# Performance work log

Hardware: AMD Instinct MI355X
Metric: run time of the kernel (lower is better)

## Reference

```python
import jax, jax.numpy as jnp
import numpy as np

B, C, H, W = 16, 512, 64, 64


def setup_inputs() -> dict:
    key = jax.random.key(0)
    ks = jax.random.split(key, 8)
    s = 1.0 / np.sqrt(C)  # fan-in scale like torch conv default
    return {
        "x": jax.random.normal(ks[0], (B, C, H, W), dtype=jnp.float32),
        "y": jax.random.normal(ks[1], (B, C), dtype=jnp.float32),
        "wq": jax.random.normal(ks[2], (C, C), dtype=jnp.float32) * s,
        "bq": jax.random.normal(ks[3], (C,), dtype=jnp.float32) * s,
        "wk": jax.random.normal(ks[4], (C, C), dtype=jnp.float32) * s,
        "bk": jax.random.normal(ks[5], (C,), dtype=jnp.float32) * s,
        "wv": jax.random.normal(ks[6], (C, C), dtype=jnp.float32) * s,
        "bv": jax.random.normal(ks[7], (C,), dtype=jnp.float32) * s,
        "gamma": jnp.ones((1,), dtype=jnp.float32),
    }


def _conv1x1_flat(inp_flat, w, b):
    # inp_flat: (B, C, N); 1x1 conv == per-pixel channel GEMM
    return jnp.einsum("oc,bcn->bon", w, inp_flat) + b[None, :, None]


def reference(x, y, wq, bq, wk, bk, wv, bv, gamma):
    b, c, h, w = x.shape
    n = h * w
    # align=True: y (B, C) broadcast to (B, C, H, W); flatten spatial dims
    y_flat = jnp.broadcast_to(y[:, :, None], (b, c, n))
    x_flat = x.reshape(b, c, n)
    # exchange=False: q = y, k = v = x
    pq = _conv1x1_flat(y_flat, wq, bq)          # (B, C, N)
    pk = _conv1x1_flat(x_flat, wk, bk)          # (B, C, N)
    pv = _conv1x1_flat(x_flat, wv, bv)          # (B, C, N)
    energy = jnp.einsum("bcn,bdn->bcd", pq, pk)  # (B, C, C) channel attention
    attn = jax.nn.softmax(energy, axis=-1)
    out = jnp.einsum("bcd,bdn->bcn", attn, pv)   # (B, C, N)
    out = out.reshape(b, c, h, w)
    return gamma * out + x
```

## Files before the change

kernel.cpp:

```cpp
#include <hip/hip_runtime.h>
#include <hip/hip_bf16.h>

#define Bn 16
#define Cn 512
#define Nn 4096

typedef unsigned short u16;
typedef __bf16 bf16x8 __attribute__((ext_vector_type(8)));
typedef float f32x4 __attribute__((ext_vector_type(4)));
typedef unsigned short u16x8 __attribute__((ext_vector_type(8)));

__device__ __forceinline__ u16 f2bf(float f) {
    __hip_bfloat16 h = __float2bfloat16(f);
    return *reinterpret_cast<u16*>(&h);
}

__device__ __forceinline__ void glds16(const u16* g, u16* l) {
    __builtin_amdgcn_global_load_lds(
        (const __attribute__((address_space(1))) void*)g,
        (__attribute__((address_space(3))) void*)l, 16, 0, 0);
}

__global__ __launch_bounds__(256) void k_transpose(
    const float* __restrict__ x, u16* __restrict__ xt, float* __restrict__ sxp)
{
    __shared__ float tile[128 * 65];
    const int b = blockIdx.z, c0 = blockIdx.y * 128, n0 = blockIdx.x * 64;
    const int t = threadIdx.x;
    const float* xb = x + ((size_t)(b * Cn + c0)) * Nn + n0;

    float part[8];
#pragma unroll
    for (int r = 0; r < 8; ++r) {
        int cl = (t >> 4) + r * 16;
        int nl = (t & 15) * 4;
        float4 v = *(const float4*)(xb + (size_t)cl * Nn + nl);
        float* tp = &tile[cl * 65 + nl];
        tp[0] = v.x; tp[1] = v.y; tp[2] = v.z; tp[3] = v.w;
        part[r] = (v.x + v.y) + (v.z + v.w);
    }
#pragma unroll
    for (int m = 1; m < 16; m <<= 1) {
#pragma unroll
        for (int r = 0; r < 8; ++r) part[r] += __shfl_xor(part[r], m);
    }
    if ((t & 15) == 0) {
#pragma unroll
        for (int r = 0; r < 8; ++r) {
            int cl = (t >> 4) + r * 16;
            sxp[(size_t)(b * Cn + c0 + cl) * 64 + blockIdx.x] = part[r];
        }
    }
    __syncthreads();
    u16* xtb = xt + ((size_t)(b * Nn + n0)) * Cn + c0;
#pragma unroll
    for (int r = 0; r < 4; ++r) {
        int nl = (t >> 4) + r * 16;
        int c8 = (t & 15) * 8;
        u16x8 hv;
#pragma unroll
        for (int i = 0; i < 8; ++i) hv[i] = f2bf(tile[(c8 + i) * 65 + nl]);
        *(u16x8*)(xtb + (size_t)nl * Cn + c8) = hv;
    }
}

__global__ __launch_bounds__(256) void k_sxred(
    const float* __restrict__ sxp, float* __restrict__ sx)
{
    int i = blockIdx.x * 256 + threadIdx.x;
    const float4* p = (const float4*)(sxp + (size_t)i * 64);
    float s = 0.f;
#pragma unroll
    for (int j = 0; j < 16; ++j) {
        float4 v = p[j];
        s += (v.x + v.y) + (v.z + v.w);
    }
    sx[i] = s;
}

__global__ __launch_bounds__(256) void k_qk(
    const float* __restrict__ wq, const float* __restrict__ bq,
    const float* __restrict__ wk, const float* __restrict__ bk,
    const float* __restrict__ y, const float* __restrict__ sx,
    float* __restrict__ qy, float* __restrict__ sk)
{
    const int w = threadIdx.x >> 6, lane = threadIdx.x & 63;
    const int o = blockIdx.x * 4 + w;
    const int b = blockIdx.y;
    const int mode = blockIdx.z;
    const float* W = mode ? wk : wq;
    const float* vec = mode ? (sx + b * Cn) : (y + b * Cn);
    float sum = 0.f;
#pragma unroll
    for (int i = 0; i < 8; ++i) {
        int k2 = lane + i * 64;
        sum += W[(size_t)o * Cn + k2] * vec[k2];
    }
#pragma unroll
    for (int m = 1; m < 64; m <<= 1) sum += __shfl_xor(sum, m);
    if (lane == 0) {
        if (mode) sk[b * Cn + o] = sum + 4096.0f * bk[o];
        else      qy[b * Cn + o] = sum + bq[o];
    }
}

__global__ __launch_bounds__(256) void k_wvt(
    const float* __restrict__ wv, u16* __restrict__ wvt)
{
    __shared__ float tl[64 * 65];
    const int d0 = blockIdx.x * 64, e0 = blockIdx.y * 64;
    const int t = threadIdx.x;
#pragma unroll
    for (int r = 0; r < 4; ++r) {
        int d = (t >> 4) + r * 16, e4 = (t & 15) * 4;
        float4 v = *(const float4*)(wv + (size_t)(d0 + d) * Cn + e0 + e4);
        float* p = &tl[d * 65 + e4];
        p[0] = v.x; p[1] = v.y; p[2] = v.z; p[3] = v.w;
    }
    __syncthreads();
#pragma unroll
    for (int r = 0; r < 4; ++r) {
        int e = (t >> 4) + r * 16, d4 = (t & 15) * 4;
        ushort4 h;
        h.x = f2bf(tl[(d4 + 0) * 65 + e]);
        h.y = f2bf(tl[(d4 + 1) * 65 + e]);
        h.z = f2bf(tl[(d4 + 2) * 65 + e]);
        h.w = f2bf(tl[(d4 + 3) * 65 + e]);
        *(ushort4*)(wvt + (size_t)(e0 + e) * Cn + d0 + d4) = h;
    }
}

__global__ __launch_bounds__(256) void k_softmax(
    const float* __restrict__ qy, const float* __restrict__ sk,
    const float* __restrict__ bv, u16* __restrict__ attn,
    float* __restrict__ beff)
{
    __shared__ float red[4], red2[4], red3[4];
    const int b = blockIdx.x >> 9, c = blockIdx.x & 511;
    const int t = threadIdx.x;
    const float q = qy[b * Cn + c];
    const float l0 = q * sk[b * Cn + t];
    const float l1 = q * sk[b * Cn + t + 256];
    float mx = fmaxf(l0, l1);
#pragma unroll
    for (int m = 1; m < 64; m <<= 1) mx = fmaxf(mx, __shfl_xor(mx, m));
    if ((t & 63) == 0) red[t >> 6] = mx;
    __syncthreads();
    mx = fmaxf(fmaxf(red[0], red[1]), fmaxf(red[2], red[3]));
    const float e0 = __expf(l0 - mx), e1 = __expf(l1 - mx);
    float s = e0 + e1;
#pragma unroll
    for (int m = 1; m < 64; m <<= 1) s += __shfl_xor(s, m);
    if ((t & 63) == 0) red2[t >> 6] = s;
    __syncthreads();
    s = red2[0] + red2[1] + red2[2] + red2[3];
    const float inv = 1.0f / s;
    const float a0 = e0 * inv, a1 = e1 * inv;
    u16* arow = attn + ((size_t)(b * Cn + c)) * Cn;
    arow[t] = f2bf(a0);
    arow[t + 256] = f2bf(a1);
    float pb = a0 * bv[t] + a1 * bv[t + 256];
#pragma unroll
    for (int m = 1; m < 64; m <<= 1) pb += __shfl_xor(pb, m);
    if ((t & 63) == 0) red3[t >> 6] = pb;
    __syncthreads();
    if (t == 0) beff[b * Cn + c] = red3[0] + red3[1] + red3[2] + red3[3];
}

template <int FINAL>
__global__ __launch_bounds__(256) void k_gemm(
    const u16* __restrict__ A, size_t strideA,
    const u16* __restrict__ Bt, size_t strideB,
    int N,
    u16* __restrict__ outBf, size_t strideOb,
    float* __restrict__ outF,
    const float* __restrict__ xres,
    const float* __restrict__ beff,
    const float* __restrict__ gamma)
{
    constexpr int K = 512;
    __shared__ u16 la[128 * 32];
    __shared__ u16 lb[128 * 32];
    const int b = blockIdx.z;
    const int m0 = blockIdx.y * 128;
    const int n0 = blockIdx.x * 128;
    A  += (size_t)b * strideA;
    Bt += (size_t)b * strideB;
    const int t = threadIdx.x;
    const int lane = t & 63;
    const int w = t >> 6;
    const int wm = (w >> 1) * 64, wn = (w & 1) * 64;
    const int l15 = lane & 15, quad = lane >> 4;

    f32x4 acc[4][4];
#pragma unroll
    for (int i = 0; i < 4; ++i)
#pragma unroll
        for (int j = 0; j < 4; ++j)
            acc[i][j] = (f32x4){0.f, 0.f, 0.f, 0.f};

    const int rb = w * 16;
    const int lrow = lane >> 2;
    const int lcol = (lane & 3) * 8;

    for (int k0 = 0; k0 < K; k0 += 32) {
        __syncthreads();
        const u16* gA = A + (size_t)(m0 + rb + lrow) * K + k0 + lcol;
        glds16(gA, &la[rb * 32]);
        glds16(gA + (size_t)64 * K, &la[(rb + 64) * 32]);
        const u16* gB = Bt + (size_t)(n0 + rb + lrow) * K + k0 + lcol;
        glds16(gB, &lb[rb * 32]);
        glds16(gB + (size_t)64 * K, &lb[(rb + 64) * 32]);
        __syncthreads();

        bf16x8 af[4], bfr[4];
#pragma unroll
        for (int mi = 0; mi < 4; ++mi)
            af[mi] = *(const bf16x8*)&la[(wm + mi * 16 + l15) * 32 + quad * 8];
#pragma unroll
        for (int ni = 0; ni < 4; ++ni)
            bfr[ni] = *(const bf16x8*)&lb[(wn + ni * 16 + l15) * 32 + quad * 8];
#pragma unroll
        for (int mi = 0; mi < 4; ++mi)
#pragma unroll
            for (int ni = 0; ni < 4; ++ni)
                acc[mi][ni] = __builtin_amdgcn_mfma_f32_16x16x32_bf16(
                    af[mi], bfr[ni], acc[mi][ni], 0, 0, 0);
    }

    if (FINAL) {
        const float g = gamma[0];
#pragma unroll
        for (int mi = 0; mi < 4; ++mi) {
#pragma unroll
            for (int reg = 0; reg < 4; ++reg) {
                const int r = m0 + wm + mi * 16 + quad * 4 + reg;
                const float be = beff[b * Cn + r];
                const size_t base = ((size_t)(b * Cn + r)) * N;
#pragma unroll
                for (int ni = 0; ni < 4; ++ni) {
                    const int cidx = n0 + wn + ni * 16 + l15;
                    outF[base + cidx] = g * (acc[mi][ni][reg] + be) + xres[base + cidx];
                }
            }
        }
    } else {
#pragma unroll
        for (int mi = 0; mi < 4; ++mi) {
#pragma unroll
            for (int reg = 0; reg < 4; ++reg) {
                const int r = m0 + wm + mi * 16 + quad * 4 + reg;
                const size_t base = (size_t)b * strideOb + (size_t)r * N;
#pragma unroll
                for (int ni = 0; ni < 4; ++ni) {
                    const int cidx = n0 + wn + ni * 16 + l15;
                    outBf[base + cidx] = f2bf(acc[mi][ni][reg]);
                }
            }
        }
    }
}

extern "C" void kernel_launch(void* const* d_in, const int* in_sizes, int n_in,
                              void* d_out, int out_size, void* d_ws, size_t ws_size,
                              hipStream_t stream)
{
    const float* x     = (const float*)d_in[0];
    const float* y     = (const float*)d_in[1];
    const float* wq    = (const float*)d_in[2];
    const float* bq    = (const float*)d_in[3];
    const float* wk    = (const float*)d_in[4];
    const float* bk    = (const float*)d_in[5];
    const float* wv    = (const float*)d_in[6];
    const float* bv    = (const float*)d_in[7];
    const float* gamma = (const float*)d_in[8];
    float* out = (float*)d_out;

    char* ws = (char*)d_ws;
    u16*   xt   = (u16*)  (ws + 0);
    float* sxp  = (float*)(ws + 67108864);
    float* sx   = (float*)(ws + 69206016);
    float* qy   = (float*)(ws + 69238784);
    float* sk   = (float*)(ws + 69271552);
    float* beff = (float*)(ws + 69304320);
    u16*   attn = (u16*)  (ws + 69337088);
    u16*   wvt  = (u16*)  (ws + 77725696);
    u16*   weff = (u16*)  (ws + 78249984);

    k_transpose<<<dim3(64, 4, Bn), dim3(256), 0, stream>>>(x, xt, sxp);
    k_sxred<<<dim3(32), dim3(256), 0, stream>>>(sxp, sx);
    k_wvt<<<dim3(8, 8), dim3(256), 0, stream>>>(wv, wvt);
    k_qk<<<dim3(128, Bn, 2), dim3(256), 0, stream>>>(wq, bq, wk, bk, y, sx, qy, sk);
    k_softmax<<<dim3(Bn * Cn), dim3(256), 0, stream>>>(qy, sk, bv, attn, beff);
    k_gemm<0><<<dim3(4, 4, Bn), dim3(256), 0, stream>>>(
        attn, (size_t)Cn * Cn, wvt, (size_t)0, Cn,
        weff, (size_t)Cn * Cn, nullptr, nullptr, nullptr, nullptr);
    k_gemm<1><<<dim3(32, 4, Bn), dim3(256), 0, stream>>>(
        weff, (size_t)Cn * Cn, xt, (size_t)Nn * Cn, Nn,
        nullptr, (size_t)0, out, x, beff, gamma);
}
```

Before: 361.1 us.

## Double K-tile depth with XOR-swizzled LDS and stage final epilogue through LDS

```diff
diff --git a/kernel.cpp b/kernel.cpp
--- a/kernel.cpp
+++ b/kernel.cpp
@@ -179,8 +179,9 @@
     const float* __restrict__ gamma)
 {
     constexpr int K = 512;
-    __shared__ u16 la[128 * 32];
-    __shared__ u16 lb[128 * 32];
+    __shared__ float smem_f[8448];
+    u16* la = (u16*)smem_f;
+    u16* lb = la + 128 * 64;
     const int b = blockIdx.z;
     const int m0 = blockIdx.y * 128;
     const int n0 = blockIdx.x * 128;
@@ -199,49 +200,78 @@
         for (int j = 0; j < 4; ++j)
             acc[i][j] = (f32x4){0.f, 0.f, 0.f, 0.f};
 
-    const int rb = w * 16;
-    const int lrow = lane >> 2;
-    const int lcol = (lane & 3) * 8;
-
-    for (int k0 = 0; k0 < K; k0 += 32) {
+    const int srow8 = lane >> 3;
+    const int lgcol = ((lane & 7) ^ srow8) * 8;
+
+    for (int k0 = 0; k0 < K; k0 += 64) {
         __syncthreads();
-        const u16* gA = A + (size_t)(m0 + rb + lrow) * K + k0 + lcol;
-        glds16(gA, &la[rb * 32]);
-        glds16(gA + (size_t)64 * K, &la[(rb + 64) * 32]);
-        const u16* gB = Bt + (size_t)(n0 + rb + lrow) * K + k0 + lcol;
-        glds16(gB, &lb[rb * 32]);
-        glds16(gB + (size_t)64 * K, &lb[(rb + 64) * 32]);
+#pragma unroll
+        for (int j = 0; j < 4; ++j) {
+            const int row = w * 32 + j * 8 + srow8;
+            const int sb = (w * 256 + j * 64) * 8;
+            glds16(A  + (size_t)(m0 + row) * K + k0 + lgcol, la + sb);
+            glds16(Bt + (size_t)(n0 + row) * K + k0 + lgcol, lb + sb);
+        }
         __syncthreads();
 
-        bf16x8 af[4], bfr[4];
-#pragma unroll
-        for (int mi = 0; mi < 4; ++mi)
-            af[mi] = *(const bf16x8*)&la[(wm + mi * 16 + l15) * 32 + quad * 8];
-#pragma unroll
-        for (int ni = 0; ni < 4; ++ni)
-            bfr[ni] = *(const bf16x8*)&lb[(wn + ni * 16 + l15) * 32 + quad * 8];
-#pragma unroll
-        for (int mi = 0; mi < 4; ++mi)
-#pragma unroll
-            for (int ni = 0; ni < 4; ++ni)
-                acc[mi][ni] = __builtin_amdgcn_mfma_f32_16x16x32_bf16(
-                    af[mi], bfr[ni], acc[mi][ni], 0, 0, 0);
+#pragma unroll
+        for (int kk2 = 0; kk2 < 2; ++kk2) {
+            bf16x8 af[4], bfr[4];
+#pragma unroll
+            for (int mi = 0; mi < 4; ++mi) {
+                const int r = wm + mi * 16 + l15;
+                const int pg = ((kk2 << 2) + quad) ^ (l15 & 7);
+                af[mi] = *(const bf16x8*)&la[r * 64 + pg * 8];
+            }
+#pragma unroll
+            for (int ni = 0; ni < 4; ++ni) {
+                const int r = wn + ni * 16 + l15;
+                const int pg = ((kk2 << 2) + quad) ^ (l15 & 7);
+                bfr[ni] = *(const bf16x8*)&lb[r * 64 + pg * 8];
+            }
+#pragma unroll
+            for (int mi = 0; mi < 4; ++mi)
+#pragma unroll
+                for (int ni = 0; ni < 4; ++ni)
+                    acc[mi][ni] = __builtin_amdgcn_mfma_f32_16x16x32_bf16(
+                        af[mi], bfr[ni], acc[mi][ni], 0, 0, 0);
+        }
     }
 
     if (FINAL) {
         const float g = gamma[0];
-#pragma unroll
-        for (int mi = 0; mi < 4; ++mi) {
-#pragma unroll
-            for (int reg = 0; reg < 4; ++reg) {
-                const int r = m0 + wm + mi * 16 + quad * 4 + reg;
+        float* lc = smem_f;
+#pragma unroll
+        for (int h = 0; h < 2; ++h) {
+            __syncthreads();
+            if ((w >> 1) == h) {
+#pragma unroll
+                for (int mi = 0; mi < 4; ++mi)
+#pragma unroll
+                    for (int reg = 0; reg < 4; ++reg) {
+                        const int rl = mi * 16 + quad * 4 + reg;
+#pragma unroll
+                        for (int ni = 0; ni < 4; ++ni)
+                            lc[rl * 132 + wn + ni * 16 + l15] = acc[mi][ni][reg];
+                    }
+            }
+            __syncthreads();
+            const int rb = h * 64;
+#pragma unroll
+            for (int rr = 0; rr < 8; ++rr) {
+                const int rl = rr * 8 + (t >> 5);
+                const int c4 = (t & 31) * 4;
+                float4 v = *(float4*)&lc[rl * 132 + c4];
+                const int r = m0 + rb + rl;
                 const float be = beff[b * Cn + r];
-                const size_t base = ((size_t)(b * Cn + r)) * N;
-#pragma unroll
-                for (int ni = 0; ni < 4; ++ni) {
-                    const int cidx = n0 + wn + ni * 16 + l15;
-                    outF[base + cidx] = g * (acc[mi][ni][reg] + be) + xres[base + cidx];
-                }
+                const size_t base = ((size_t)(b * Cn + r)) * N + n0 + c4;
+                float4 xr = *(const float4*)(xres + base);
+                float4 o;
+                o.x = g * (v.x + be) + xr.x;
+                o.y = g * (v.y + be) + xr.y;
+                o.z = g * (v.z + be) + xr.z;
+                o.w = g * (v.w + be) + xr.w;
+                *(float4*)(outF + base) = o;
             }
         }
     } else {
```

Result: faster. 351.6 us (-2.6%).
